# Optimization experiments

Measured on AMD Instinct MI355X. Metric: run time of the kernel, lower is better.

The kernel has to match this reference:

```python
import jax, jax.numpy as jnp
import numpy as np

N = 50000
E = 800000
IN_DIM = 128
OUT_DIM = 128
EDGE_DIM = 3
H = 4
HD = OUT_DIM // H  # 32
SCALE = HD ** -0.5


def setup_inputs() -> dict:
    key = jax.random.key(0)
    ks = jax.random.split(key, 10)
    x = jax.random.normal(ks[0], (N, IN_DIM), dtype=jnp.float32)
    edge_index = jax.random.randint(ks[1], (2, E), 0, N, dtype=jnp.int64)
    edge_attr = jax.random.normal(ks[2], (E, EDGE_DIM), dtype=jnp.float32)
    s = 1.0 / np.sqrt(IN_DIM)
    Wq = jax.random.normal(ks[3], (IN_DIM, H * HD), dtype=jnp.float32) * s
    Wk = jax.random.normal(ks[4], (IN_DIM, H * HD), dtype=jnp.float32) * s
    Wv = jax.random.normal(ks[5], (IN_DIM, H * HD), dtype=jnp.float32) * s
    We = jax.random.normal(ks[6], (EDGE_DIM, H), dtype=jnp.float32) * (1.0 / np.sqrt(EDGE_DIM))
    Wo = jax.random.normal(ks[7], (H * HD, OUT_DIM), dtype=jnp.float32) * (1.0 / np.sqrt(H * HD))
    bo = jnp.zeros((OUT_DIM,), dtype=jnp.float32)
    Wm = jax.random.normal(ks[8], (IN_DIM + OUT_DIM, OUT_DIM), dtype=jnp.float32) * (1.0 / np.sqrt(IN_DIM + OUT_DIM))
    bm = jnp.zeros((OUT_DIM,), dtype=jnp.float32)
    return {"x": x, "edge_index": edge_index, "edge_attr": edge_attr,
            "Wq": Wq, "Wk": Wk, "Wv": Wv, "We": We, "Wo": Wo, "bo": bo,
            "Wm": Wm, "bm": bm}


def reference(x, edge_index, edge_attr, Wq, Wk, Wv, We, Wo, bo, Wm, bm):
    n = x.shape[0]
    src = edge_index[0]
    dst = edge_index[1]
    Q = (x @ Wq).reshape(n, H, HD)
    K = (x @ Wk).reshape(n, H, HD)
    V = (x @ Wv).reshape(n, H, HD)
    edge_bias = edge_attr @ We                                  # [E, H]
    attn = jnp.sum(Q[dst] * K[src], axis=-1) * SCALE + edge_bias  # [E, H]
    attn = jnp.where(attn >= 0, attn, 0.2 * attn)               # leaky_relu(0.2)
    # NOTE: original uses a single GLOBAL max over all edges/heads for stability
    attn_exp = jnp.exp(attn - jnp.max(attn))
    attn_sum = jax.ops.segment_sum(attn_exp, dst, num_segments=n)  # [N, H]
    attn_norm = attn_exp / jnp.maximum(attn_sum[dst], 1e-12)
    # dropout disabled (eval mode)
    weighted_V = V[src] * attn_norm[:, :, None]                 # [E, H, HD]
    agg = jax.ops.segment_sum(weighted_V, dst, num_segments=n)  # [N, H, HD]
    agg = agg.reshape(n, H * HD) @ Wo + bo                      # [N, OUT]
    h = jnp.concatenate([x, agg], axis=1) @ Wm + bm
    return jax.nn.relu(h)
```

## Files before the change

kernel.cpp:

```cpp
#include <hip/hip_runtime.h>
#include <hip/hip_bf16.h>
#include <math.h>

#define NN 50000
#define NE 800000
#define DIM 128
#define NH 4
#define HD 32
#define ATTN_SCALE 0.17677669529663687f
#define MTILE 64
#define NBK 782
#define PTS 2048
#define HBLKS 104

#define K1_QKV_BASE 104
#define K1_WXB_BASE 296
#define K1_GRID     361
#define K3_PART_N     391
#define K3_PACKO_BASE 391
#define K3_XCVT_BASE  519
#define K3_GRID       6769
#define K4_CSR_N 782
#define K4_GRID  1564
#define AO_GRID 3125

typedef unsigned int uint;
typedef unsigned short ushort;
typedef __attribute__((ext_vector_type(8))) short short8;
typedef __attribute__((ext_vector_type(4))) float f32x4;

__device__ inline ushort f2bf(float f) {
    __hip_bfloat16 h = __float2bfloat16(f);
    return *(ushort*)&h;
}
__device__ inline float bflo(uint u) { return __uint_as_float(u << 16); }
__device__ inline float bfhi(uint u) { return __uint_as_float(u & 0xffff0000u); }

__global__ __launch_bounds__(256) void k1_kernel(
    const int* __restrict__ dst, int* __restrict__ bkt_cnt,
    const float* __restrict__ Wq, const float* __restrict__ Wk,
    const float* __restrict__ Wv, short* __restrict__ BpQKV,
    const float* __restrict__ Wo, const float* __restrict__ Wm,
    const float* __restrict__ bo, const float* __restrict__ bm,
    float* __restrict__ Wx, float* __restrict__ bprime)
{
    const int bid = blockIdx.x;
    const int tid = threadIdx.x;

    if (bid < HBLKS) {
        __shared__ int c[NBK];
        for (int l = tid; l < NBK; l += 256) c[l] = 0;
        __syncthreads();
        for (int e = bid * 256 + tid; e < NE; e += HBLKS * 256)
            atomicAdd(&c[dst[e] >> 6], 1);
        __syncthreads();
        for (int l = tid; l < NBK; l += 256)
            if (c[l]) atomicAdd(&bkt_cnt[l], c[l]);
    } else if (bid < K1_WXB_BASE) {
        const int idx = (bid - K1_QKV_BASE) * 256 + tid;
        const int j = idx & 7, lane = (idx >> 3) & 63;
        const int rest = idx >> 9;
        const int nt = rest % 24, kc = rest / 24;
        const int k = kc * 32 + (lane >> 4) * 8 + j;
        const int n = nt * 16 + (lane & 15);
        const float* W = (n < 128) ? Wq : (n < 256 ? Wk : Wv);
        BpQKV[idx] = (short)f2bf(W[k * 128 + (n & 127)]);
    } else {
        const int r = (bid - K1_WXB_BASE) * 2 + (tid >> 7);
        const int j = tid & 127;
        if (r < 128) {
            float acc = 0.f;
            for (int t = 0; t < 128; ++t)
                acc = fmaf(Wo[r * 128 + t], Wm[(128 + t) * 128 + j], acc);
            Wx[r * 128 + j] = acc;
        } else if (r == 128) {
            float acc = bm[j];
            for (int t = 0; t < 128; ++t)
                acc = fmaf(bo[t], Wm[(128 + t) * 128 + j], acc);
            bprime[j] = acc;
        }
    }
}

__global__ __launch_bounds__(256) void bkt_scan_kernel(
    const int* __restrict__ bkt_cnt,
    int* __restrict__ bkt_base, int* __restrict__ bkt_cursor,
    int* __restrict__ rowptr)
{
    __shared__ int part[256];
    const int tid = threadIdx.x;
    const int b0 = tid * 4;
    int v0 = 0, v1 = 0, v2 = 0, v3 = 0;
    if (b0 + 0 < NBK) v0 = bkt_cnt[b0 + 0];
    if (b0 + 1 < NBK) v1 = bkt_cnt[b0 + 1];
    if (b0 + 2 < NBK) v2 = bkt_cnt[b0 + 2];
    if (b0 + 3 < NBK) v3 = bkt_cnt[b0 + 3];
    const int s = v0 + v1 + v2 + v3;
    part[tid] = s;
    __syncthreads();
    for (int off = 1; off < 256; off <<= 1) {
        const int y = (tid >= off) ? part[tid - off] : 0;
        __syncthreads();
        part[tid] += y;
        __syncthreads();
    }
    const int ex = part[tid] - s;
    const int r0 = ex, r1 = ex + v0, r2 = ex + v0 + v1, r3 = ex + v0 + v1 + v2;
    if (b0 + 0 < NBK) { bkt_base[b0 + 0] = r0; bkt_cursor[b0 + 0] = r0; }
    if (b0 + 1 < NBK) { bkt_base[b0 + 1] = r1; bkt_cursor[b0 + 1] = r1; }
    if (b0 + 2 < NBK) { bkt_base[b0 + 2] = r2; bkt_cursor[b0 + 2] = r2; }
    if (b0 + 3 < NBK) { bkt_base[b0 + 3] = r3; bkt_cursor[b0 + 3] = r3; }
    if (tid == 255) bkt_base[NBK] = part[255];
    if (tid == 0)   rowptr[NN] = NE;
}

__global__ __launch_bounds__(256) void k3_kernel(
    const int* __restrict__ src, const int* __restrict__ dst,
    const float* __restrict__ edge_attr, const float* __restrict__ We,
    int* __restrict__ bkt_cursor,
    uint* __restrict__ ppack, uint2* __restrict__ pebp,
    const float* __restrict__ Wm, const float* __restrict__ Wx,
    short* __restrict__ BpOut,
    const float* __restrict__ x, ushort* __restrict__ xb)
{
    const int bid = blockIdx.x;
    const int tid = threadIdx.x;

    if (bid < K3_PART_N) {
        __shared__ int cnt[NBK], rbase[NBK], cnt2[NBK];
        for (int l = tid; l < NBK; l += 256) cnt[l] = 0;
        __syncthreads();
        const int e0 = bid * PTS;
        #pragma unroll
        for (int it = 0; it < 8; ++it) {
            const int e = e0 + it * 256 + tid;
            if (e < NE) atomicAdd(&cnt[dst[e] >> 6], 1);
        }
        __syncthreads();
        for (int l = tid; l < NBK; l += 256) {
            const int c = cnt[l];
            rbase[l] = c ? atomicAdd(&bkt_cursor[l], c) : 0;
            cnt2[l] = 0;
        }
        __syncthreads();
        #pragma unroll
        for (int it = 0; it < 8; ++it) {
            const int e = e0 + it * 256 + tid;
            if (e < NE) {
                const int d = dst[e];
                const int b = d >> 6;
                const int r = atomicAdd(&cnt2[b], 1);
                const int pos = rbase[b] + r;
                ppack[pos] = (uint)src[e] | ((uint)(d & 63) << 16);
                const float a0 = edge_attr[e * 3 + 0];
                const float a1 = edge_attr[e * 3 + 1];
                const float a2 = edge_attr[e * 3 + 2];
                const float b0 = a0 * We[0] + a1 * We[4] + a2 * We[8];
                const float b1 = a0 * We[1] + a1 * We[5] + a2 * We[9];
                const float b2 = a0 * We[2] + a1 * We[6] + a2 * We[10];
                const float b3 = a0 * We[3] + a1 * We[7] + a2 * We[11];
                uint2 ep;
                ep.x = (uint)f2bf(b0) | ((uint)f2bf(b1) << 16);
                ep.y = (uint)f2bf(b2) | ((uint)f2bf(b3) << 16);
                pebp[pos] = ep;
            }
        }
    } else if (bid < K3_XCVT_BASE) {
        const int idx = (bid - K3_PACKO_BASE) * 256 + tid;
        const int j = idx & 7, lane = (idx >> 3) & 63;
        const int rest = idx >> 9;
        const int nt = rest & 7, kc = rest >> 3;
        const int k = kc * 32 + (lane >> 4) * 8 + j;
        const int n = nt * 16 + (lane & 15);
        const float v = (k < 128) ? Wm[k * 128 + n] : Wx[(k - 128) * 128 + n];
        BpOut[idx] = (short)f2bf(v);
    } else {
        const int i = (bid - K3_XCVT_BASE) * 256 + tid;
        const float4 v = ((const float4*)x)[i];
        ushort4 o;
        o.x = f2bf(v.x); o.y = f2bf(v.y); o.z = f2bf(v.z); o.w = f2bf(v.w);
        ((ushort4*)xb)[i] = o;
    }
}

__global__ __launch_bounds__(256) void k4_kernel(
    const int* __restrict__ bkt_base,
    const uint* __restrict__ ppack, const uint2* __restrict__ pebp,
    int* __restrict__ rowptr, uint4* __restrict__ edata,
    const ushort* __restrict__ xb, const short* __restrict__ BpQKV,
    ushort* __restrict__ Qb, ushort* __restrict__ KVb)
{
    const int bid = blockIdx.x;
    const int tid = threadIdx.x;

    if (bid < K4_CSR_N) {
        __shared__ int cnt[64];
        __shared__ int pre[64];
        const int base = bkt_base[bid];
        const int n = bkt_base[bid + 1] - base;
        const int node0 = bid << 6;

        if (tid < 64) cnt[tid] = 0;
        __syncthreads();
        for (int i = base + tid; i < base + n; i += 256)
            atomicAdd(&cnt[ppack[i] >> 16], 1);
        __syncthreads();

        if (tid < 64) {
            const int c = cnt[tid];
            int xsc = c;
            #pragma unroll
            for (int off = 1; off < 64; off <<= 1) {
                const int y = __shfl_up(xsc, off);
                if (tid >= off) xsc += y;
            }
            const int ex = base + xsc - c;
            pre[tid] = ex;
            const int g = node0 + tid;
            if (g < NN) rowptr[g] = ex;
        }
        __syncthreads();

        for (int i = base + tid; i < base + n; i += 256) {
            const uint v = ppack[i];
            const int pos = atomicAdd(&pre[v >> 16], 1);
            const uint2 ep = pebp[i];
            uint4 rec;
            rec.x = v & 0xFFFFu;
            rec.y = ep.x;
            rec.z = ep.y;
            rec.w = 0u;
            edata[pos] = rec;
        }
    } else {
        const int qb = bid - K4_CSR_N;
        const int wave = tid >> 6;
        const int lane = tid & 63;
        const int m = lane & 15, quad = lane >> 4;
        const int row0w = qb * MTILE + wave * 16;
        const int arow = row0w + m;
        const bool rowok = arow < NN;

        short8 a[4];
        #pragma unroll
        for (int kc = 0; kc < 4; ++kc)
            a[kc] = rowok ? *(const short8*)(xb + (size_t)arow * 128 + kc * 32 + quad * 8)
                          : (short8)(0);

        const int NT = 24;
        for (int nt = 0; nt < NT; nt += 2) {
            f32x4 acc0 = {0.f, 0.f, 0.f, 0.f}, acc1 = {0.f, 0.f, 0.f, 0.f};
            #pragma unroll
            for (int kc = 0; kc < 4; ++kc) {
                const short8 b0 = *(const short8*)(BpQKV + ((size_t)(kc * NT + nt) * 64 + lane) * 8);
                const short8 b1 = *(const short8*)(BpQKV + ((size_t)(kc * NT + nt + 1) * 64 + lane) * 8);
                acc0 = __builtin_amdgcn_mfma_f32_16x16x32_bf16(a[kc], b0, acc0, 0, 0, 0);
                acc1 = __builtin_amdgcn_mfma_f32_16x16x32_bf16(a[kc], b1, acc1, 0, 0, 0);
            }
            #pragma unroll
            for (int t = 0; t < 2; ++t) {
                const f32x4 acc = t ? acc1 : acc0;
                const int c = (nt + t) * 16 + m;
                #pragma unroll
                for (int g = 0; g < 4; ++g) {
                    const int r = row0w + quad * 4 + g;
                    if (r < NN) {
                        if (c < 128) Qb[(size_t)r * 128 + c] = f2bf(acc[g]);
                        else        KVb[(size_t)r * 256 + (c - 128)] = f2bf(acc[g]);
                    }
                }
            }
        }
    }
}

__global__ __launch_bounds__(1024) void attn_out_kernel(
    const ushort* __restrict__ Qb, const ushort* __restrict__ KVb,
    const int* __restrict__ rowptr, const uint4* __restrict__ edata,
    const ushort* __restrict__ xb, const short* __restrict__ BpOut,
    const float* __restrict__ bprime, float* __restrict__ out)
{
    __shared__ ushort sagg[16][136];
    const int tid = threadIdx.x;
    const int wv = tid >> 6;
    const int lane = tid & 63;
    const int node0 = blockIdx.x * 16;

    {
        const int d = node0 + wv;
        const int g = lane >> 4;
        const int t = lane & 15;
        const int h = t >> 2;
        const int begin = rowptr[d];
        const int end   = rowptr[d + 1];

        const uint4 uq = *(const uint4*)(Qb + (size_t)d * DIM + 8 * t);
        const float q0 = bflo(uq.x), q1 = bfhi(uq.x);
        const float q2 = bflo(uq.y), q3 = bfhi(uq.y);
        const float q4 = bflo(uq.z), q5 = bfhi(uq.z);
        const float q6 = bflo(uq.w), q7 = bfhi(uq.w);

        float ss = 0.f;
        float a0 = 0.f, a1 = 0.f, a2 = 0.f, a3 = 0.f;
        float a4 = 0.f, a5 = 0.f, a6 = 0.f, a7 = 0.f;

        if (begin < end) {
            int ec = begin + g;
            if (ec >= end) ec = end - 1;
            uint4 rec = edata[ec];

            for (int p = begin; p < end; p += 4) {
                const bool ok = (p + g) < end;
                const int pn = p + 4;
                uint4 recn = rec;
                if (pn < end) {
                    int en = pn + g;
                    if (en >= end) en = end - 1;
                    recn = edata[en];
                }

                const int s = (int)rec.x;
                const uint wrd = (h & 2) ? rec.z : rec.y;
                const float eb = (h & 1) ? bfhi(wrd) : bflo(wrd);

                const ushort* kv = KVb + (size_t)s * 256 + 8 * t;
                const uint4 uk = *(const uint4*)(kv);
                const uint4 uv = *(const uint4*)(kv + 128);

                float da = q0 * bflo(uk.x);
                float db = q1 * bfhi(uk.x);
                da = fmaf(q2, bflo(uk.y), da);
                db = fmaf(q3, bfhi(uk.y), db);
                da = fmaf(q4, bflo(uk.z), da);
                db = fmaf(q5, bfhi(uk.z), db);
                da = fmaf(q6, bflo(uk.w), da);
                db = fmaf(q7, bfhi(uk.w), db);
                float part = da + db;
                part += __shfl_xor(part, 1);
                part += __shfl_xor(part, 2);

                float a = fmaf(part, ATTN_SCALE, eb);
                a = (a >= 0.f) ? a : 0.2f * a;
                const float w = ok ? __expf(a) : 0.f;

                ss += w;
                a0 = fmaf(w, bflo(uv.x), a0);
                a1 = fmaf(w, bfhi(uv.x), a1);
                a2 = fmaf(w, bflo(uv.y), a2);
                a3 = fmaf(w, bfhi(uv.y), a3);
                a4 = fmaf(w, bflo(uv.z), a4);
                a5 = fmaf(w, bfhi(uv.z), a5);
                a6 = fmaf(w, bflo(uv.w), a6);
                a7 = fmaf(w, bfhi(uv.w), a7);

                rec = recn;
            }
        }

        ss += __shfl_xor(ss, 16);
        ss += __shfl_xor(ss, 32);
        a0 += __shfl_xor(a0, 16); a0 += __shfl_xor(a0, 32);
        a1 += __shfl_xor(a1, 16); a1 += __shfl_xor(a1, 32);
        a2 += __shfl_xor(a2, 16); a2 += __shfl_xor(a2, 32);
        a3 += __shfl_xor(a3, 16); a3 += __shfl_xor(a3, 32);
        a4 += __shfl_xor(a4, 16); a4 += __shfl_xor(a4, 32);
        a5 += __shfl_xor(a5, 16); a5 += __shfl_xor(a5, 32);
        a6 += __shfl_xor(a6, 16); a6 += __shfl_xor(a6, 32);
        a7 += __shfl_xor(a7, 16); a7 += __shfl_xor(a7, 32);

        if (g == 0) {
            const float inv = 1.f / fmaxf(ss, 1e-12f);
            uint4 o;
            o.x = (uint)f2bf(a0 * inv) | ((uint)f2bf(a1 * inv) << 16);
            o.y = (uint)f2bf(a2 * inv) | ((uint)f2bf(a3 * inv) << 16);
            o.z = (uint)f2bf(a4 * inv) | ((uint)f2bf(a5 * inv) << 16);
            o.w = (uint)f2bf(a6 * inv) | ((uint)f2bf(a7 * inv) << 16);
            *(uint4*)(&sagg[wv][8 * t]) = o;
        }
    }

    __syncthreads();

    if (wv < 8) {
        const int m = lane & 15, quad = lane >> 4;
        const int arow = node0 + m;

        short8 a[8];
        #pragma unroll
        for (int kc = 0; kc < 4; ++kc)
            a[kc] = *(const short8*)(xb + (size_t)arow * 128 + kc * 32 + quad * 8);
        #pragma unroll
        for (int kc = 0; kc < 4; ++kc)
            a[4 + kc] = *(const short8*)(&sagg[m][kc * 32 + quad * 8]);

        const int NT = 8;
        const int nt = wv;
        f32x4 acc = {0.f, 0.f, 0.f, 0.f};
        #pragma unroll
        for (int kc = 0; kc < 8; ++kc) {
            const short8 b0 = *(const short8*)(BpOut + ((size_t)(kc * NT + nt) * 64 + lane) * 8);
            acc = __builtin_amdgcn_mfma_f32_16x16x32_bf16(a[kc], b0, acc, 0, 0, 0);
        }
        const int c = nt * 16 + m;
        const float bb = bprime[c];
        #pragma unroll
        for (int g2 = 0; g2 < 4; ++g2) {
            const int r = node0 + quad * 4 + g2;
            out[(size_t)r * 128 + c] = fmaxf(acc[g2] + bb, 0.f);
        }
    }
}

extern "C" void kernel_launch(void* const* d_in, const int* in_sizes, int n_in,
                              void* d_out, int out_size, void* d_ws, size_t ws_size,
                              hipStream_t stream)
{
    const float* x         = (const float*)d_in[0];
    const int*   edge_idx  = (const int*)d_in[1];
    const float* edge_attr = (const float*)d_in[2];
    const float* Wq        = (const float*)d_in[3];
    const float* Wk        = (const float*)d_in[4];
    const float* Wv        = (const float*)d_in[5];
    const float* We        = (const float*)d_in[6];
    const float* Wo        = (const float*)d_in[7];
    const float* bo        = (const float*)d_in[8];
    const float* Wm        = (const float*)d_in[9];
    const float* bm        = (const float*)d_in[10];
    float* out = (float*)d_out;

    const int* src = edge_idx;
    const int* dst = edge_idx + NE;

    ushort* xb   = (ushort*)d_ws;
    ushort* Qb   = xb + (size_t)NN * DIM;
    ushort* KVb  = Qb + (size_t)NN * DIM;
    uint*  ppack = (uint*)(KVb + (size_t)NN * 2 * DIM);
    uint2* pebp  = (uint2*)(ppack + NE);
    uint4* edata = (uint4*)(pebp + NE);
    float* Wx    = (float*)(edata + NE);
    float* bprime= Wx + 16384;
    short* BpQKV = (short*)(bprime + 128);
    short* BpOut = BpQKV + 49152;
    int*   rowptr= (int*)(BpOut + 32768);
    int*   bkt_cnt    = rowptr + 50048;
    int*   bkt_base   = bkt_cnt + 800;
    int*   bkt_cursor = bkt_base + 800;

    hipMemsetAsync(bkt_cnt, 0, NBK * sizeof(int), stream);

    k1_kernel<<<K1_GRID, 256, 0, stream>>>(
        dst, bkt_cnt, Wq, Wk, Wv, BpQKV, Wo, Wm, bo, bm, Wx, bprime);

    bkt_scan_kernel<<<1, 256, 0, stream>>>(bkt_cnt, bkt_base, bkt_cursor, rowptr);

    k3_kernel<<<K3_GRID, 256, 0, stream>>>(
        src, dst, edge_attr, We, bkt_cursor, ppack, pebp, Wm, Wx, BpOut, x, xb);

    k4_kernel<<<K4_GRID, 256, 0, stream>>>(
        bkt_base, ppack, pebp, rowptr, edata, xb, BpQKV, Qb, KVb);

    attn_out_kernel<<<AO_GRID, 1024, 0, stream>>>(
        Qb, KVb, rowptr, edata, xb, BpOut, bprime, out);
}
```

Before: 243.7 us.

## Use 32-node blocks with dynamic per-wave node queue in attention-output kernel

The attention-output kernel now handles 32 destination nodes per 1024-thread block instead of 16. Its 16 waves pull node tasks from an LDS atomic counter, so waves that finish short adjacency lists early take more nodes. All 16 waves then run the output MFMA, two row tiles by eight column tiles, and the x tile load is hoisted ahead of the gather phase. This is meant to balance uneven node degrees within a block and keep every wave busy in the GEMM stage, at the cost of an atomic per task and bounds checks for the partial last block.

```diff
diff --git a/kernel.cpp b/kernel.cpp
--- a/kernel.cpp
+++ b/kernel.cpp
@@ -22,7 +22,8 @@
 #define K3_GRID       6769
 #define K4_CSR_N 782
 #define K4_GRID  1564
-#define AO_GRID 3125
+#define AO_NODES 32
+#define AO_GRID  1563
 
 typedef unsigned int uint;
 typedef unsigned short ushort;
@@ -280,121 +281,141 @@
     const ushort* __restrict__ xb, const short* __restrict__ BpOut,
     const float* __restrict__ bprime, float* __restrict__ out)
 {
-    __shared__ ushort sagg[16][136];
+    __shared__ ushort sagg[AO_NODES][136];
+    __shared__ int q_next;
     const int tid = threadIdx.x;
     const int wv = tid >> 6;
     const int lane = tid & 63;
-    const int node0 = blockIdx.x * 16;
+    const int node0 = blockIdx.x * AO_NODES;
+
+    const int m = lane & 15, quad = lane >> 4;
+    const int tile = wv >> 3;
+    const int nt = wv & 7;
+    const int arow2 = node0 + tile * 16 + m;
+    short8 ax[4];
+    #pragma unroll
+    for (int kc = 0; kc < 4; ++kc)
+        ax[kc] = (arow2 < NN)
+            ? *(const short8*)(xb + (size_t)arow2 * 128 + kc * 32 + quad * 8)
+            : (short8)(0);
+
+    if (tid == 0) q_next = 0;
+    __syncthreads();
 
     {
-        const int d = node0 + wv;
         const int g = lane >> 4;
         const int t = lane & 15;
         const int h = t >> 2;
-        const int begin = rowptr[d];
-        const int end   = rowptr[d + 1];
-
-        const uint4 uq = *(const uint4*)(Qb + (size_t)d * DIM + 8 * t);
-        const float q0 = bflo(uq.x), q1 = bfhi(uq.x);
-        const float q2 = bflo(uq.y), q3 = bfhi(uq.y);
-        const float q4 = bflo(uq.z), q5 = bfhi(uq.z);
-        const float q6 = bflo(uq.w), q7 = bfhi(uq.w);
-
-        float ss = 0.f;
-        float a0 = 0.f, a1 = 0.f, a2 = 0.f, a3 = 0.f;
-        float a4 = 0.f, a5 = 0.f, a6 = 0.f, a7 = 0.f;
-
-        if (begin < end) {
-            int ec = begin + g;
-            if (ec >= end) ec = end - 1;
-            uint4 rec = edata[ec];
-
-            for (int p = begin; p < end; p += 4) {
-                const bool ok = (p + g) < end;
-                const int pn = p + 4;
-                uint4 recn = rec;
-                if (pn < end) {
-                    int en = pn + g;
-                    if (en >= end) en = end - 1;
-                    recn = edata[en];
+
+        for (;;) {
+            int task = 0;
+            if (lane == 0) task = atomicAdd(&q_next, 1);
+            task = __shfl(task, 0);
+            if (task >= AO_NODES) break;
+            const int d = node0 + task;
+
+            float ss = 0.f;
+            float a0 = 0.f, a1 = 0.f, a2 = 0.f, a3 = 0.f;
+            float a4 = 0.f, a5 = 0.f, a6 = 0.f, a7 = 0.f;
+
+            if (d < NN) {
+                const int begin = rowptr[d];
+                const int end   = rowptr[d + 1];
+
+                const uint4 uq = *(const uint4*)(Qb + (size_t)d * DIM + 8 * t);
+                const float q0 = bflo(uq.x), q1 = bfhi(uq.x);
+                const float q2 = bflo(uq.y), q3 = bfhi(uq.y);
+                const float q4 = bflo(uq.z), q5 = bfhi(uq.z);
+                const float q6 = bflo(uq.w), q7 = bfhi(uq.w);
+
+                if (begin < end) {
+                    int ec = begin + g;
+                    if (ec >= end) ec = end - 1;
+                    uint4 rec = edata[ec];
+
+                    for (int p = begin; p < end; p += 4) {
+                        const bool ok = (p + g) < end;
+                        const int pn = p + 4;
+                        uint4 recn = rec;
+                        if (pn < end) {
+                            int en = pn + g;
+                            if (en >= end) en = end - 1;
+                            recn = edata[en];
+                        }
+
+                        const int s = (int)rec.x;
+                        const uint wrd = (h & 2) ? rec.z : rec.y;
+                        const float eb = (h & 1) ? bfhi(wrd) : bflo(wrd);
+
+                        const ushort* kv = KVb + (size_t)s * 256 + 8 * t;
+                        const uint4 uk = *(const uint4*)(kv);
+                        const uint4 uv = *(const uint4*)(kv + 128);
+
+                        float da = q0 * bflo(uk.x);
+                        float db = q1 * bfhi(uk.x);
+                        da = fmaf(q2, bflo(uk.y), da);
+                        db = fmaf(q3, bfhi(uk.y), db);
+                        da = fmaf(q4, bflo(uk.z), da);
+                        db = fmaf(q5, bfhi(uk.z), db);
+                        da = fmaf(q6, bflo(uk.w), da);
+                        db = fmaf(q7, bfhi(uk.w), db);
+                        float part = da + db;
+                        part += __shfl_xor(part, 1);
+                        part += __shfl_xor(part, 2);
+
+                        float a = fmaf(part, ATTN_SCALE, eb);
+                        a = (a >= 0.f) ? a : 0.2f * a;
+                        const float w = ok ? __expf(a) : 0.f;
+
+                        ss += w;
+                        a0 = fmaf(w, bflo(uv.x), a0);
+                        a1 = fmaf(w, bfhi(uv.x), a1);
+                        a2 = fmaf(w, bflo(uv.y), a2);
+                        a3 = fmaf(w, bfhi(uv.y), a3);
+                        a4 = fmaf(w, bflo(uv.z), a4);
+                        a5 = fmaf(w, bfhi(uv.z), a5);
+                        a6 = fmaf(w, bflo(uv.w), a6);
+                        a7 = fmaf(w, bfhi(uv.w), a7);
+
+                        rec = recn;
+                    }
                 }
-
-                const int s = (int)rec.x;
-                const uint wrd = (h & 2) ? rec.z : rec.y;
-                const float eb = (h & 1) ? bfhi(wrd) : bflo(wrd);
-
-                const ushort* kv = KVb + (size_t)s * 256 + 8 * t;
-                const uint4 uk = *(const uint4*)(kv);
-                const uint4 uv = *(const uint4*)(kv + 128);
-
-                float da = q0 * bflo(uk.x);
-                float db = q1 * bfhi(uk.x);
-                da = fmaf(q2, bflo(uk.y), da);
-                db = fmaf(q3, bfhi(uk.y), db);
-                da = fmaf(q4, bflo(uk.z), da);
-                db = fmaf(q5, bfhi(uk.z), db);
-                da = fmaf(q6, bflo(uk.w), da);
-                db = fmaf(q7, bfhi(uk.w), db);
-                float part = da + db;
-                part += __shfl_xor(part, 1);
-                part += __shfl_xor(part, 2);
-
-                float a = fmaf(part, ATTN_SCALE, eb);
-                a = (a >= 0.f) ? a : 0.2f * a;
-                const float w = ok ? __expf(a) : 0.f;
-
-                ss += w;
-                a0 = fmaf(w, bflo(uv.x), a0);
-                a1 = fmaf(w, bfhi(uv.x), a1);
-                a2 = fmaf(w, bflo(uv.y), a2);
-                a3 = fmaf(w, bfhi(uv.y), a3);
-                a4 = fmaf(w, bflo(uv.z), a4);
-                a5 = fmaf(w, bfhi(uv.z), a5);
-                a6 = fmaf(w, bflo(uv.w), a6);
-                a7 = fmaf(w, bfhi(uv.w), a7);
-
-                rec = recn;
-            }
-        }
-
-        ss += __shfl_xor(ss, 16);
-        ss += __shfl_xor(ss, 32);
-        a0 += __shfl_xor(a0, 16); a0 += __shfl_xor(a0, 32);
-        a1 += __shfl_xor(a1, 16); a1 += __shfl_xor(a1, 32);
-        a2 += __shfl_xor(a2, 16); a2 += __shfl_xor(a2, 32);
-        a3 += __shfl_xor(a3, 16); a3 += __shfl_xor(a3, 32);
-        a4 += __shfl_xor(a4, 16); a4 += __shfl_xor(a4, 32);
-        a5 += __shfl_xor(a5, 16); a5 += __shfl_xor(a5, 32);
-        a6 += __shfl_xor(a6, 16); a6 += __shfl_xor(a6, 32);
-        a7 += __shfl_xor(a7, 16); a7 += __shfl_xor(a7, 32);
-
-        if (g == 0) {
-            const float inv = 1.f / fmaxf(ss, 1e-12f);
-            uint4 o;
-            o.x = (uint)f2bf(a0 * inv) | ((uint)f2bf(a1 * inv) << 16);
-            o.y = (uint)f2bf(a2 * inv) | ((uint)f2bf(a3 * inv) << 16);
-            o.z = (uint)f2bf(a4 * inv) | ((uint)f2bf(a5 * inv) << 16);
-            o.w = (uint)f2bf(a6 * inv) | ((uint)f2bf(a7 * inv) << 16);
-            *(uint4*)(&sagg[wv][8 * t]) = o;
+            }
+
+            ss += __shfl_xor(ss, 16);
+            ss += __shfl_xor(ss, 32);
+            a0 += __shfl_xor(a0, 16); a0 += __shfl_xor(a0, 32);
+            a1 += __shfl_xor(a1, 16); a1 += __shfl_xor(a1, 32);
+            a2 += __shfl_xor(a2, 16); a2 += __shfl_xor(a2, 32);
+            a3 += __shfl_xor(a3, 16); a3 += __shfl_xor(a3, 32);
+            a4 += __shfl_xor(a4, 16); a4 += __shfl_xor(a4, 32);
+            a5 += __shfl_xor(a5, 16); a5 += __shfl_xor(a5, 32);
+            a6 += __shfl_xor(a6, 16); a6 += __shfl_xor(a6, 32);
+            a7 += __shfl_xor(a7, 16); a7 += __shfl_xor(a7, 32);
+
+            if (g == 0) {
+                const float inv = 1.f / fmaxf(ss, 1e-12f);
+                uint4 o;
+                o.x = (uint)f2bf(a0 * inv) | ((uint)f2bf(a1 * inv) << 16);
+                o.y = (uint)f2bf(a2 * inv) | ((uint)f2bf(a3 * inv) << 16);
+                o.z = (uint)f2bf(a4 * inv) | ((uint)f2bf(a5 * inv) << 16);
+                o.w = (uint)f2bf(a6 * inv) | ((uint)f2bf(a7 * inv) << 16);
+                *(uint4*)(&sagg[task][8 * t]) = o;
+            }
         }
     }
 
     __syncthreads();
 
-    if (wv < 8) {
-        const int m = lane & 15, quad = lane >> 4;
-        const int arow = node0 + m;
-
+    {
         short8 a[8];
         #pragma unroll
+        for (int kc = 0; kc < 4; ++kc) a[kc] = ax[kc];
+        #pragma unroll
         for (int kc = 0; kc < 4; ++kc)
-            a[kc] = *(const short8*)(xb + (size_t)arow * 128 + kc * 32 + quad * 8);
-        #pragma unroll
-        for (int kc = 0; kc < 4; ++kc)
-            a[4 + kc] = *(const short8*)(&sagg[m][kc * 32 + quad * 8]);
+            a[4 + kc] = *(const short8*)(&sagg[tile * 16 + m][kc * 32 + quad * 8]);
 
         const int NT = 8;
-        const int nt = wv;
         f32x4 acc = {0.f, 0.f, 0.f, 0.f};
         #pragma unroll
         for (int kc = 0; kc < 8; ++kc) {
@@ -405,8 +426,8 @@
         const float bb = bprime[c];
         #pragma unroll
         for (int g2 = 0; g2 < 4; ++g2) {
-            const int r = node0 + quad * 4 + g2;
-            out[(size_t)r * 128 + c] = fmaxf(acc[g2] + bb, 0.f);
+            const int r = node0 + tile * 16 + quad * 4 + g2;
+            if (r < NN) out[(size_t)r * 128 + c] = fmaxf(acc[g2] + bb, 0.f);
         }
     }
 }
```

After: 270.3 us. 10.9% more time.
